# Kernel optimization log

Hardware: AMD Instinct MI355X
Metric: run time of the kernel (lower is better)

Reference implementation:

```python
import jax, jax.numpy as jnp
from jax import lax
import numpy as np

# inferred ssconv semantics (custom CUDA kernel not in source):
#  - input x: (B, H, W, Cin) channels-last, Cin = per-pixel channel count
#  - in_index: (B, H, W) in [0, IN_GROUPS): routes each input pixel's Cin channels
#    to the corresponding slice of the weight's input-channel dim (gather/scatter MoE-style dispatch)
#  - weight: (OUT_GROUPS*Cout, IN_GROUPS*Cin, kh, kw), bias: (OUT_GROUPS*Cout,)
#  - per output pixel, one out-group is selected (maxout over groups); the kernel
#    returns both the selected Cout channels and the winning group index (out_index)

IN_GROUPS = 4
OUT_GROUPS = 4
STRIDE = 1  # pad = stride//2 in the wrapper; output (H-1)//s+1 == SAME padding


def setup_inputs() -> dict:
    key = jax.random.key(0)
    k1, k2, k3, k4 = jax.random.split(key, 4)
    x = jax.random.normal(k1, (8, 256, 256, 16), dtype=jnp.float32)
    in_index = jax.random.randint(k2, (8, 256, 256), 0, IN_GROUPS, dtype=jnp.int32)
    weight = jax.random.normal(k3, (64, 64, 3, 3), dtype=jnp.float32) * 0.05
    bias = jax.random.normal(k4, (64,), dtype=jnp.float32) * 0.05
    return {"x": x, "in_index": in_index, "weight": weight, "bias": bias}


def reference(x, in_index, weight, bias):
    B, H, W, Cin = x.shape
    OC, IC, kh, kw = weight.shape  # OC = OUT_GROUPS*Cout, IC = IN_GROUPS*Cin
    Cout = OC // OUT_GROUPS

    # dispatch: scatter each pixel's channels into its in-group slice (rest zero)
    onehot = jax.nn.one_hot(in_index, IN_GROUPS, dtype=x.dtype)          # (B,H,W,G)
    x_full = (onehot[..., :, None] * x[..., None, :]).reshape(B, H, W, IN_GROUPS * Cin)

    # dense conv over the dispatched tensor == per-pixel gathered group weights
    w_hwio = jnp.transpose(weight, (2, 3, 1, 0))  # (kh,kw,IC,OC)
    out = lax.conv_general_dilated(
        x_full, w_hwio, window_strides=(STRIDE, STRIDE), padding="SAME",
        dimension_numbers=("NHWC", "HWIO", "NHWC"))
    out = out + bias  # (B,H',W',OC)

    Bo, Ho, Wo, _ = out.shape
    out_g = out.reshape(Bo, Ho, Wo, OUT_GROUPS, Cout)
    scores = out_g.max(axis=-1)                    # (B,H',W',G) per-group response
    out_index = jnp.argmax(scores, axis=-1)        # winning out-group per pixel
    sel = jnp.take_along_axis(out_g, out_index[..., None, None], axis=3)
    sel = jnp.squeeze(sel, axis=3)                 # (B,H',W',Cout)
    return sel, out_index.astype(jnp.int32)
```

## Files before the change

### kernel.cpp

```cpp
#include <hip/hip_runtime.h>

#define H 256
#define W 256
#define BATCH 8
#define CIN 16
#define TW 64
#define TH 4
#define HWC (TW + 2)
#define HHC (TH + 2)
#define NHALO (HWC * HHC)
#define PSTR 24
#define FIX_CAP 16384
#define GAP_TAU 1e-3f

#define OFF_HS   19008
#define OFF_GS   38016
#define OFF_BB   39600
#define SMEM_BYTES 72368

typedef __attribute__((ext_vector_type(8))) short short8;
typedef __attribute__((ext_vector_type(8))) _Float16 half8;
typedef __attribute__((ext_vector_type(4))) float f32x4;

union S8H8 { short8 s; half8 h; };
__device__ __forceinline__ half8 as_h8(short8 s) { S8H8 u; u.s = s; return u.h; }
union HU { _Float16 h; unsigned short u; };

__device__ __forceinline__ void gload_lds16(const void* g, void* l) {
    __builtin_amdgcn_global_load_lds(
        (const __attribute__((address_space(1))) unsigned int*)g,
        (__attribute__((address_space(3))) unsigned int*)l, 16, 0, 0);
}

__device__ __forceinline__ float4 add4(float4 a, float4 b) {
    return make_float4(a.x + b.x, a.y + b.y, a.z + b.z, a.w + b.w);
}
__device__ __forceinline__ float max4(float4 a) {
    return fmaxf(fmaxf(a.x, a.y), fmaxf(a.z, a.w));
}

__global__ void wprep_kernel(const float* __restrict__ w, unsigned short* __restrict__ wt) {
    int i = blockIdx.x * 256 + threadIdx.x;
    if (i >= 73728) return;
    int k   = i & 63;
    int n   = (i >> 6) & 63;
    int sel = (i >> 12) & 1;
    int tap = i >> 13;
    float v = w[(n * 64 + k) * 9 + tap] * 64.0f;
    HU uh; uh.h = (_Float16)v;
    unsigned short ob;
    if (sel == 0) {
        ob = uh.u;
    } else {
        _Float16 lo = (_Float16)((v - (float)uh.h) * 2048.0f);
        HU us; us.h = (_Float16)(uh.h + lo);
        ob = us.u;
    }
    int ksw = k ^ ((n & 7) << 3);
    wt[(((tap * 2 + sel) * 64) + n) * 64 + ksw] = ob;
}

#define CVT(F, VH, VS, J) { HU uh_; uh_.h = (_Float16)(F); \
    _Float16 lo_ = (_Float16)(((F) - (float)uh_.h) * 2048.0f); \
    HU us_; us_.h = (_Float16)(uh_.h + lo_); \
    VH[J] = (short)uh_.u; VS[J] = (short)us_.u; }

__global__ __launch_bounds__(256, 2) void ssconv_mfma_kernel(
    const float* __restrict__ x, const int* __restrict__ gidx,
    const unsigned short* __restrict__ wt, const float* __restrict__ bias,
    float* __restrict__ out_sel, float* __restrict__ out_idx,
    unsigned* __restrict__ fix_cnt, unsigned* __restrict__ fix_list)
{
    __shared__ __align__(16) char smem[SMEM_BYTES];
    unsigned short* hHi  = (unsigned short*)smem;
    unsigned short* hS   = (unsigned short*)(smem + OFF_HS);
    int* gsL             = (int*)(smem + OFF_GS);
    unsigned short* bufB = (unsigned short*)(smem + OFF_BB);
    float* outS          = (float*)smem;

    const int tid  = threadIdx.x;
    const int x0   = blockIdx.x * TW;
    const int y0   = blockIdx.y * TH;
    const int bz   = blockIdx.z;
    const int wvid = tid >> 6;
    const int L    = tid & 63;
    const int q    = L >> 4;
    const int lm   = L & 15;
    const int c0   = (q & 1) * 8;

#pragma unroll
    for (int c = 0; c < 4; ++c) {
        int seg = wvid * 4 + c;
        gload_lds16((const char*)wt + seg * 1024 + L * 16,
                    (char*)bufB + seg * 1024);
    }

    for (int i = tid; i < NHALO; i += 256) {
        int r = i / HWC, c = i % HWC;
        int hy = y0 + r - 1, hx = x0 + c - 1;
        bool ok = (hy >= 0) && (hy < H) && (hx >= 0) && (hx < W);
        float4 a0 = make_float4(0, 0, 0, 0), a1 = a0, a2 = a0, a3 = a0;
        int g = 0;
        if (ok) {
            const float4* src = (const float4*)(x + (((size_t)bz * H + hy) * W + hx) * CIN);
            a0 = src[0]; a1 = src[1]; a2 = src[2]; a3 = src[3];
            g = gidx[((size_t)bz * H + hy) * W + hx];
        }
        gsL[i] = g;
        short8 vh0, vs0, vh1, vs1;
        CVT(a0.x, vh0, vs0, 0) CVT(a0.y, vh0, vs0, 1) CVT(a0.z, vh0, vs0, 2) CVT(a0.w, vh0, vs0, 3)
        CVT(a1.x, vh0, vs0, 4) CVT(a1.y, vh0, vs0, 5) CVT(a1.z, vh0, vs0, 6) CVT(a1.w, vh0, vs0, 7)
        CVT(a2.x, vh1, vs1, 0) CVT(a2.y, vh1, vs1, 1) CVT(a2.z, vh1, vs1, 2) CVT(a2.w, vh1, vs1, 3)
        CVT(a3.x, vh1, vs1, 4) CVT(a3.y, vh1, vs1, 5) CVT(a3.z, vh1, vs1, 6) CVT(a3.w, vh1, vs1, 7)
        *(short8*)&hHi[i * PSTR + 0] = vh0;
        *(short8*)&hHi[i * PSTR + 8] = vh1;
        *(short8*)&hS[i * PSTR + 0]  = vs0;
        *(short8*)&hS[i * PSTR + 8]  = vs1;
    }
    __syncthreads();

    f32x4 acch[4][4] = {};
    f32x4 accc[4][4] = {};

#pragma unroll 1
    for (int tap = 0; tap < 9; ++tap) {
        if (tap < 8) {
            const char* gsrc = (const char*)(wt + (size_t)(tap + 1) * 8192);
            char* ldst = (char*)bufB + ((tap + 1) & 1) * 16384;
#pragma unroll
            for (int c = 0; c < 4; ++c) {
                int seg = wvid * 4 + c;
                gload_lds16(gsrc + seg * 1024 + L * 16, ldst + seg * 1024);
            }
        }
        const unsigned short* bb = bufB + (tap & 1) * 8192;

        const int dy = tap / 3, dx = tap % 3;
        const int hbase = (wvid + dy) * HWC + lm + dx;

        short8 ah[4], aS[4];
        int gg[4];
#pragma unroll
        for (int m = 0; m < 4; ++m) {
            int hb = hbase + 16 * m;
            gg[m] = gsL[hb];
            ah[m] = *(const short8*)&hHi[hb * PSTR + c0];
            aS[m] = *(const short8*)&hS[hb * PSTR + c0];
        }

#pragma unroll
        for (int ks = 0; ks < 2; ++ks) {
            const int gk = ks * 2 + (q >> 1);
            const int kcol = (ks * 32 + q * 8) ^ ((lm & 7) << 3);
            short8 bh[4], bt[4];
#pragma unroll
            for (int nt = 0; nt < 4; ++nt) {
                bh[nt] = *(const short8*)&bb[(nt * 16 + lm) * 64 + kcol];
                bt[nt] = *(const short8*)&bb[(64 + nt * 16 + lm) * 64 + kcol];
            }
            const short8 z = (short8)0;
#pragma unroll
            for (int m = 0; m < 4; ++m) {
                bool mm = (gg[m] == gk);
                short8 a0 = mm ? ah[m] : z;
                short8 s0 = mm ? aS[m] : z;
#pragma unroll
                for (int nt = 0; nt < 4; ++nt) {
                    acch[m][nt] = __builtin_amdgcn_mfma_f32_16x16x32_f16(as_h8(a0), as_h8(bh[nt]), acch[m][nt], 0, 0, 0);
                    accc[m][nt] = __builtin_amdgcn_mfma_f32_16x16x32_f16(as_h8(s0), as_h8(bt[nt]), accc[m][nt], 0, 0, 0);
                }
            }
        }
        __syncthreads();
    }

    const float SHm = 2047.0f / 131072.0f;
    const float SLc = 1.0f / 131072.0f;
#pragma unroll
    for (int m = 0; m < 4; ++m)
#pragma unroll
        for (int nt = 0; nt < 4; ++nt)
#pragma unroll
            for (int r = 0; r < 4; ++r) {
                int xcol = 16 * m + q * 4 + r;
                outS[wvid * 4352 + xcol * 68 + nt * 16 + lm] =
                    acch[m][nt][r] * SHm + accc[m][nt][r] * SLc;
            }
    __syncthreads();

#pragma unroll 1
    for (int pp = 0; pp < 2; ++pp) {
        int p  = (tid >> 1) + pp * 128;
        int hh = tid & 1;
        int pw = p >> 6, px_ = p & 63;
        const float4* srcp = (const float4*)(outS + pw * 4352 + px_ * 68 + hh * 32);
        const float4* bb2 = (const float4*)(bias + hh * 32);
        float4 r0 = add4(srcp[0], bb2[0]), r1 = add4(srcp[1], bb2[1]);
        float4 r2 = add4(srcp[2], bb2[2]), r3 = add4(srcp[3], bb2[3]);
        float4 r4 = add4(srcp[4], bb2[4]), r5 = add4(srcp[5], bb2[5]);
        float4 r6 = add4(srcp[6], bb2[6]), r7 = add4(srcp[7], bb2[7]);

        float ma = fmaxf(fmaxf(max4(r0), max4(r1)), fmaxf(max4(r2), max4(r3)));
        float mb = fmaxf(fmaxf(max4(r4), max4(r5)), fmaxf(max4(r6), max4(r7)));
        float pa = __shfl_xor(ma, 1, 64);
        float pb = __shfl_xor(mb, 1, 64);
        float s0, s1, s2, s3;
        if (hh == 0) { s0 = ma; s1 = mb; s2 = pa; s3 = pb; }
        else         { s0 = pa; s1 = pb; s2 = ma; s3 = mb; }
        int bg = 0; float best = s0;
        if (s1 > best) { best = s1; bg = 1; }
        if (s2 > best) { best = s2; bg = 2; }
        if (s3 > best) { best = s3; bg = 3; }

        int gy = y0 + pw, gx = x0 + px_;
        size_t opix = ((size_t)bz * H + gy) * W + gx;
        if ((bg >> 1) == hh) {
            bool useB = (bg & 1) != 0;
            float4 o0 = useB ? r4 : r0, o1 = useB ? r5 : r1;
            float4 o2 = useB ? r6 : r2, o3 = useB ? r7 : r3;
            float4* os = (float4*)(out_sel + opix * 16);
            os[0] = o0; os[1] = o1; os[2] = o2; os[3] = o3;
        }
        if (hh == 0) {
            out_idx[opix] = (float)bg;
            float o1v = (bg == 0) ? s1 : s0;
            float o2v = (bg <= 1) ? s2 : s1;
            float o3v = (bg <= 2) ? s3 : s2;
            float second = fmaxf(o1v, fmaxf(o2v, o3v));
            if (best - second < GAP_TAU) {
                unsigned slot = atomicAdd(fix_cnt, 1u);
                if (slot < FIX_CAP) fix_list[slot] = (unsigned)opix;
            }
        }
    }
}

__global__ void fixup_kernel(const float* __restrict__ x, const int* __restrict__ gidx,
                             const float* __restrict__ w, const float* __restrict__ bias,
                             float* __restrict__ out_sel, float* __restrict__ out_idx,
                             const unsigned* __restrict__ fix_cnt,
                             const unsigned* __restrict__ fix_list)
{
    unsigned n = *fix_cnt;
    if (n > FIX_CAP) n = FIX_CAP;
    const int lane = threadIdx.x & 63;
    const int nwaves = gridDim.x * (blockDim.x >> 6);
    unsigned widx = blockIdx.x * (blockDim.x >> 6) + (threadIdx.x >> 6);

    for (; widx < n; widx += nwaves) {
        unsigned opix = fix_list[widx];
        int b  = opix >> 16;
        int y  = (opix >> 8) & 255;
        int xc = opix & 255;
        double acc = (double)bias[lane];
        for (int dy = 0; dy < 3; ++dy) {
            int yy = y + dy - 1;
            if (yy < 0 || yy >= H) continue;
            for (int dx = 0; dx < 3; ++dx) {
                int xx = xc + dx - 1;
                if (xx < 0 || xx >= W) continue;
                size_t pix = ((size_t)b * H + yy) * W + xx;
                int g = gidx[pix];
                const float* xp = x + pix * 16;
                const float* wp = w + (size_t)(lane * 64 + g * 16) * 9 + (dy * 3 + dx);
#pragma unroll
                for (int c = 0; c < 16; ++c)
                    acc = fma((double)wp[c * 9], (double)xp[c], acc);
            }
        }
        double m = acc;
        m = fmax(m, __shfl_xor(m, 1, 64));
        m = fmax(m, __shfl_xor(m, 2, 64));
        m = fmax(m, __shfl_xor(m, 4, 64));
        m = fmax(m, __shfl_xor(m, 8, 64));
        double g0 = __shfl(m, 0, 64), g1 = __shfl(m, 16, 64);
        double g2 = __shfl(m, 32, 64), g3 = __shfl(m, 48, 64);
        int bg = 0; double bb = g0;
        if (g1 > bb) { bb = g1; bg = 1; }
        if (g2 > bb) { bb = g2; bg = 2; }
        if (g3 > bb) { bb = g3; bg = 3; }
        if ((lane >> 4) == bg) out_sel[(size_t)opix * 16 + (lane & 15)] = (float)acc;
        if (lane == 0) out_idx[opix] = (float)bg;
    }
}

extern "C" void kernel_launch(void* const* d_in, const int* in_sizes, int n_in,
                              void* d_out, int out_size, void* d_ws, size_t ws_size,
                              hipStream_t stream) {
    const float* x    = (const float*)d_in[0];
    const int*   gidx = (const int*)d_in[1];
    const float* w    = (const float*)d_in[2];
    const float* bias = (const float*)d_in[3];

    unsigned short* wt = (unsigned short*)d_ws;
    unsigned* fix_cnt  = (unsigned*)((char*)d_ws + 147456);
    unsigned* fix_list = (unsigned*)((char*)d_ws + 147472);

    float* out_sel = (float*)d_out;
    float* out_idx = (float*)d_out + (size_t)BATCH * H * W * CIN;

    hipMemsetAsync(fix_cnt, 0, 16, stream);
    wprep_kernel<<<288, 256, 0, stream>>>(w, wt);

    dim3 grid(W / TW, H / TH, BATCH);
    ssconv_mfma_kernel<<<grid, 256, 0, stream>>>(x, gidx, wt, bias, out_sel, out_idx,
                                                 fix_cnt, fix_list);
    fixup_kernel<<<256, 256, 0, stream>>>(x, gidx, w, bias, out_sel, out_idx,
                                          fix_cnt, fix_list);
}
```

Before: 189.0 us.

## Switch split-precision conv from fp16 MFMA to int8 hi/lo MFMA with per-tile scaling

Replaces the two-term fp16 decomposition with a two-term int8 quantization: weights get per-output-channel scales and activations get a per-tile absmax scale, and the conv runs on i32 16x16x64 int8 MFMA using three products (hi*hi, hi*lo, lo*hi). The tile height doubles to 8 rows with 512 threads, and all nine weight taps are preloaded into LDS at once instead of double-buffered. Group masking now uses a single K=64 step per tap. The memset is folded into the weight-prep kernel and the near-tie threshold is widened. The aim is to use the higher int8 MFMA throughput and cut LDS traffic, at the cost of accuracy and possibly more pixels sent to the fp64 fixup.

```diff
diff --git a/kernel.cpp b/kernel.cpp
--- a/kernel.cpp
+++ b/kernel.cpp
@@ -5,26 +5,22 @@
 #define BATCH 8
 #define CIN 16
 #define TW 64
-#define TH 4
+#define TH 8
 #define HWC (TW + 2)
 #define HHC (TH + 2)
 #define NHALO (HWC * HHC)
-#define PSTR 24
 #define FIX_CAP 16384
-#define GAP_TAU 1e-3f
-
-#define OFF_HS   19008
-#define OFF_GS   38016
-#define OFF_BB   39600
-#define SMEM_BYTES 72368
-
-typedef __attribute__((ext_vector_type(8))) short short8;
-typedef __attribute__((ext_vector_type(8))) _Float16 half8;
-typedef __attribute__((ext_vector_type(4))) float f32x4;
-
-union S8H8 { short8 s; half8 h; };
-__device__ __forceinline__ half8 as_h8(short8 s) { S8H8 u; u.s = s; return u.h; }
-union HU { _Float16 h; unsigned short u; };
+#define GAP_TAU 2e-3f
+
+#define OFF_XH   73728
+#define OFF_XL   84288
+#define OFF_GS   94848
+#define OFF_SW   97488
+#define OFF_BIAS 97744
+#define OFF_RED  98000
+#define SMEM_BYTES 98032
+
+typedef __attribute__((ext_vector_type(4))) int i32x4;
 
 __device__ __forceinline__ void gload_lds16(const void* g, void* l) {
     __builtin_amdgcn_global_load_lds(
@@ -39,44 +35,52 @@
     return fmaxf(fmaxf(a.x, a.y), fmaxf(a.z, a.w));
 }
 
-__global__ void wprep_kernel(const float* __restrict__ w, unsigned short* __restrict__ wt) {
-    int i = blockIdx.x * 256 + threadIdx.x;
-    if (i >= 73728) return;
-    int k   = i & 63;
-    int n   = (i >> 6) & 63;
-    int sel = (i >> 12) & 1;
-    int tap = i >> 13;
-    float v = w[(n * 64 + k) * 9 + tap] * 64.0f;
-    HU uh; uh.h = (_Float16)v;
-    unsigned short ob;
-    if (sel == 0) {
-        ob = uh.u;
-    } else {
-        _Float16 lo = (_Float16)((v - (float)uh.h) * 2048.0f);
-        HU us; us.h = (_Float16)(uh.h + lo);
-        ob = us.u;
-    }
-    int ksw = k ^ ((n & 7) << 3);
-    wt[(((tap * 2 + sel) * 64) + n) * 64 + ksw] = ob;
-}
-
-#define CVT(F, VH, VS, J) { HU uh_; uh_.h = (_Float16)(F); \
-    _Float16 lo_ = (_Float16)(((F) - (float)uh_.h) * 2048.0f); \
-    HU us_; us_.h = (_Float16)(uh_.h + lo_); \
-    VH[J] = (short)uh_.u; VS[J] = (short)us_.u; }
-
-__global__ __launch_bounds__(256, 2) void ssconv_mfma_kernel(
+__global__ void wprep_kernel(const float* __restrict__ w, char* __restrict__ wt,
+                             float* __restrict__ sw_ws, unsigned* __restrict__ fix_cnt) {
+    const int n = blockIdx.x;
+    const int k = threadIdx.x;
+    if (n == 0 && k == 0) fix_cnt[0] = 0u;
+
+    float v[9];
+    float m = 0.f;
+#pragma unroll
+    for (int t = 0; t < 9; ++t) {
+        v[t] = w[(n * 64 + k) * 9 + t];
+        m = fmaxf(m, fabsf(v[t]));
+    }
+#pragma unroll
+    for (int s = 1; s < 64; s <<= 1) m = fmaxf(m, __shfl_xor(m, s, 64));
+    const float inv = (m > 0.f) ? (127.f / m) : 0.f;
+    if (k == 0) sw_ws[n] = m * (1.f / 127.f);
+
+    const int nt = n >> 4, nl = n & 15, kq = k >> 4, j = k & 15;
+    const int lane16 = (kq * 16 + nl) * 16 + j;
+#pragma unroll
+    for (int t = 0; t < 9; ++t) {
+        float f = v[t] * inv;
+        int h = __float2int_rn(f);
+        int l = __float2int_rn((f - (float)h) * 128.f);
+        wt[((t * 2 + 0) * 4 + nt) * 1024 + lane16] = (char)h;
+        wt[((t * 2 + 1) * 4 + nt) * 1024 + lane16] = (char)l;
+    }
+}
+
+__global__ __launch_bounds__(512, 2) void ssconv_i8_kernel(
     const float* __restrict__ x, const int* __restrict__ gidx,
-    const unsigned short* __restrict__ wt, const float* __restrict__ bias,
+    const char* __restrict__ wt, const float* __restrict__ sw_ws,
+    const float* __restrict__ bias,
     float* __restrict__ out_sel, float* __restrict__ out_idx,
     unsigned* __restrict__ fix_cnt, unsigned* __restrict__ fix_list)
 {
     __shared__ __align__(16) char smem[SMEM_BYTES];
-    unsigned short* hHi  = (unsigned short*)smem;
-    unsigned short* hS   = (unsigned short*)(smem + OFF_HS);
-    int* gsL             = (int*)(smem + OFF_GS);
-    unsigned short* bufB = (unsigned short*)(smem + OFF_BB);
-    float* outS          = (float*)smem;
+    char*  bufB  = smem;
+    char*  xhL   = smem + OFF_XH;
+    char*  xlL   = smem + OFF_XL;
+    int*   gsL   = (int*)(smem + OFF_GS);
+    float* swdL  = (float*)(smem + OFF_SW);
+    float* biasL = (float*)(smem + OFF_BIAS);
+    float* redL  = (float*)(smem + OFF_RED);
+    float* outS  = (float*)smem;
 
     const int tid  = threadIdx.x;
     const int x0   = blockIdx.x * TW;
@@ -86,152 +90,172 @@
     const int L    = tid & 63;
     const int q    = L >> 4;
     const int lm   = L & 15;
-    const int c0   = (q & 1) * 8;
-
-#pragma unroll
-    for (int c = 0; c < 4; ++c) {
-        int seg = wvid * 4 + c;
-        gload_lds16((const char*)wt + seg * 1024 + L * 16,
-                    (char*)bufB + seg * 1024);
-    }
-
-    for (int i = tid; i < NHALO; i += 256) {
-        int r = i / HWC, c = i % HWC;
-        int hy = y0 + r - 1, hx = x0 + c - 1;
-        bool ok = (hy >= 0) && (hy < H) && (hx >= 0) && (hx < W);
-        float4 a0 = make_float4(0, 0, 0, 0), a1 = a0, a2 = a0, a3 = a0;
-        int g = 0;
-        if (ok) {
-            const float4* src = (const float4*)(x + (((size_t)bz * H + hy) * W + hx) * CIN);
-            a0 = src[0]; a1 = src[1]; a2 = src[2]; a3 = src[3];
-            g = gidx[((size_t)bz * H + hy) * W + hx];
-        }
-        gsL[i] = g;
-        short8 vh0, vs0, vh1, vs1;
-        CVT(a0.x, vh0, vs0, 0) CVT(a0.y, vh0, vs0, 1) CVT(a0.z, vh0, vs0, 2) CVT(a0.w, vh0, vs0, 3)
-        CVT(a1.x, vh0, vs0, 4) CVT(a1.y, vh0, vs0, 5) CVT(a1.z, vh0, vs0, 6) CVT(a1.w, vh0, vs0, 7)
-        CVT(a2.x, vh1, vs1, 0) CVT(a2.y, vh1, vs1, 1) CVT(a2.z, vh1, vs1, 2) CVT(a2.w, vh1, vs1, 3)
-        CVT(a3.x, vh1, vs1, 4) CVT(a3.y, vh1, vs1, 5) CVT(a3.z, vh1, vs1, 6) CVT(a3.w, vh1, vs1, 7)
-        *(short8*)&hHi[i * PSTR + 0] = vh0;
-        *(short8*)&hHi[i * PSTR + 8] = vh1;
-        *(short8*)&hS[i * PSTR + 0]  = vs0;
-        *(short8*)&hS[i * PSTR + 8]  = vs1;
-    }
+
+#pragma unroll
+    for (int it = 0; it < 9; ++it)
+        gload_lds16(wt + it * 8192 + tid * 16, bufB + it * 8192 + tid * 16);
+
+    if (tid < 64) { swdL[tid] = sw_ws[tid]; biasL[tid] = bias[tid]; }
+
+    float4 av[2][4];
+    int gv[2];
+    float am = 0.f;
+#pragma unroll
+    for (int s = 0; s < 2; ++s) {
+        av[s][0] = av[s][1] = av[s][2] = av[s][3] = make_float4(0, 0, 0, 0);
+        gv[s] = 0;
+        int i = tid + s * 512;
+        if (i < NHALO) {
+            int r = i / HWC, c = i - r * HWC;
+            int hy = y0 + r - 1, hx = x0 + c - 1;
+            if (hy >= 0 && hy < H && hx >= 0 && hx < W) {
+                const float4* src = (const float4*)(x + (((size_t)bz * H + hy) * W + hx) * CIN);
+                av[s][0] = src[0]; av[s][1] = src[1]; av[s][2] = src[2]; av[s][3] = src[3];
+                gv[s] = gidx[((size_t)bz * H + hy) * W + hx];
+            }
+#pragma unroll
+            for (int j = 0; j < 4; ++j)
+                am = fmaxf(am, fmaxf(fmaxf(fabsf(av[s][j].x), fabsf(av[s][j].y)),
+                                     fmaxf(fabsf(av[s][j].z), fabsf(av[s][j].w))));
+        }
+    }
+#pragma unroll
+    for (int s = 1; s < 64; s <<= 1) am = fmaxf(am, __shfl_xor(am, s, 64));
+    if (L == 0) redL[wvid] = am;
     __syncthreads();
-
-    f32x4 acch[4][4] = {};
-    f32x4 accc[4][4] = {};
+    float bm = redL[0];
+#pragma unroll
+    for (int wv = 1; wv < 8; ++wv) bm = fmaxf(bm, redL[wv]);
+    const float qinv = (bm > 0.f) ? (127.f / bm) : 0.f;
+    const float sB   = bm * (1.f / 127.f);
+
+#pragma unroll
+    for (int s = 0; s < 2; ++s) {
+        int i = tid + s * 512;
+        if (i < NHALO) {
+            unsigned hw[4], lw[4];
+#pragma unroll
+            for (int j = 0; j < 4; ++j) {
+                float fs[4] = {av[s][j].x, av[s][j].y, av[s][j].z, av[s][j].w};
+                unsigned hword = 0, lword = 0;
+#pragma unroll
+                for (int e = 0; e < 4; ++e) {
+                    float f_ = fs[e] * qinv;
+                    int h_ = __float2int_rn(f_);
+                    int l_ = __float2int_rn((f_ - (float)h_) * 128.f);
+                    hword |= ((unsigned)(h_ & 255)) << (8 * e);
+                    lword |= ((unsigned)(l_ & 255)) << (8 * e);
+                }
+                hw[j] = hword; lw[j] = lword;
+            }
+            *(uint4*)&xhL[(size_t)i * 16] = make_uint4(hw[0], hw[1], hw[2], hw[3]);
+            *(uint4*)&xlL[(size_t)i * 16] = make_uint4(lw[0], lw[1], lw[2], lw[3]);
+            gsL[i] = gv[s];
+        }
+    }
+    __syncthreads();
+
+    i32x4 acc1[4][4] = {};
+    i32x4 acc2[4][4] = {};
 
 #pragma unroll 1
     for (int tap = 0; tap < 9; ++tap) {
-        if (tap < 8) {
-            const char* gsrc = (const char*)(wt + (size_t)(tap + 1) * 8192);
-            char* ldst = (char*)bufB + ((tap + 1) & 1) * 16384;
-#pragma unroll
-            for (int c = 0; c < 4; ++c) {
-                int seg = wvid * 4 + c;
-                gload_lds16(gsrc + seg * 1024 + L * 16, ldst + seg * 1024);
-            }
-        }
-        const unsigned short* bb = bufB + (tap & 1) * 8192;
-
-        const int dy = tap / 3, dx = tap % 3;
+        const int dy = tap / 3, dx = tap - dy * 3;
         const int hbase = (wvid + dy) * HWC + lm + dx;
-
-        short8 ah[4], aS[4];
-        int gg[4];
+        const char* bB = bufB + tap * 8192;
+
+        i32x4 bh[4], bl[4];
+#pragma unroll
+        for (int nt = 0; nt < 4; ++nt) {
+            bh[nt] = *(const i32x4*)(bB + nt * 1024 + L * 16);
+            bl[nt] = *(const i32x4*)(bB + 4096 + nt * 1024 + L * 16);
+        }
 #pragma unroll
         for (int m = 0; m < 4; ++m) {
             int hb = hbase + 16 * m;
-            gg[m] = gsL[hb];
-            ah[m] = *(const short8*)&hHi[hb * PSTR + c0];
-            aS[m] = *(const short8*)&hS[hb * PSTR + c0];
-        }
-
-#pragma unroll
-        for (int ks = 0; ks < 2; ++ks) {
-            const int gk = ks * 2 + (q >> 1);
-            const int kcol = (ks * 32 + q * 8) ^ ((lm & 7) << 3);
-            short8 bh[4], bt[4];
+            int gg = gsL[hb];
+            i32x4 ah = *(const i32x4*)&xhL[(size_t)hb * 16];
+            i32x4 al = *(const i32x4*)&xlL[(size_t)hb * 16];
+            bool keep = (gg == q);
+            i32x4 z = {};
+            i32x4 a0 = keep ? ah : z;
+            i32x4 a1 = keep ? al : z;
 #pragma unroll
             for (int nt = 0; nt < 4; ++nt) {
-                bh[nt] = *(const short8*)&bb[(nt * 16 + lm) * 64 + kcol];
-                bt[nt] = *(const short8*)&bb[(64 + nt * 16 + lm) * 64 + kcol];
-            }
-            const short8 z = (short8)0;
-#pragma unroll
-            for (int m = 0; m < 4; ++m) {
-                bool mm = (gg[m] == gk);
-                short8 a0 = mm ? ah[m] : z;
-                short8 s0 = mm ? aS[m] : z;
-#pragma unroll
-                for (int nt = 0; nt < 4; ++nt) {
-                    acch[m][nt] = __builtin_amdgcn_mfma_f32_16x16x32_f16(as_h8(a0), as_h8(bh[nt]), acch[m][nt], 0, 0, 0);
-                    accc[m][nt] = __builtin_amdgcn_mfma_f32_16x16x32_f16(as_h8(s0), as_h8(bt[nt]), accc[m][nt], 0, 0, 0);
+                acc1[m][nt] = __builtin_amdgcn_mfma_i32_16x16x64_i8(a0, bh[nt], acc1[m][nt], 0, 0, 0);
+                acc2[m][nt] = __builtin_amdgcn_mfma_i32_16x16x64_i8(a0, bl[nt], acc2[m][nt], 0, 0, 0);
+                acc2[m][nt] = __builtin_amdgcn_mfma_i32_16x16x64_i8(a1, bh[nt], acc2[m][nt], 0, 0, 0);
+            }
+        }
+    }
+    __syncthreads();
+
+    float swb[4];
+#pragma unroll
+    for (int nt = 0; nt < 4; ++nt) swb[nt] = sB * swdL[nt * 16 + lm];
+
+#pragma unroll
+    for (int pass = 0; pass < 2; ++pass) {
+#pragma unroll
+        for (int mh = 0; mh < 2; ++mh) {
+            const int m = pass * 2 + mh;
+            const int prow = wvid * 32 + mh * 16 + q * 4;
+#pragma unroll
+            for (int nt = 0; nt < 4; ++nt)
+#pragma unroll
+                for (int r = 0; r < 4; ++r) {
+                    float v = swb[nt] *
+                              ((float)acc1[m][nt][r] + (float)acc2[m][nt][r] * (1.f / 128.f));
+                    outS[(prow + r) * 68 + nt * 16 + lm] = v;
                 }
-            }
         }
         __syncthreads();
-    }
-
-    const float SHm = 2047.0f / 131072.0f;
-    const float SLc = 1.0f / 131072.0f;
-#pragma unroll
-    for (int m = 0; m < 4; ++m)
-#pragma unroll
-        for (int nt = 0; nt < 4; ++nt)
-#pragma unroll
-            for (int r = 0; r < 4; ++r) {
-                int xcol = 16 * m + q * 4 + r;
-                outS[wvid * 4352 + xcol * 68 + nt * 16 + lm] =
-                    acch[m][nt][r] * SHm + accc[m][nt][r] * SLc;
-            }
-    __syncthreads();
-
-#pragma unroll 1
-    for (int pp = 0; pp < 2; ++pp) {
-        int p  = (tid >> 1) + pp * 128;
-        int hh = tid & 1;
-        int pw = p >> 6, px_ = p & 63;
-        const float4* srcp = (const float4*)(outS + pw * 4352 + px_ * 68 + hh * 32);
-        const float4* bb2 = (const float4*)(bias + hh * 32);
-        float4 r0 = add4(srcp[0], bb2[0]), r1 = add4(srcp[1], bb2[1]);
-        float4 r2 = add4(srcp[2], bb2[2]), r3 = add4(srcp[3], bb2[3]);
-        float4 r4 = add4(srcp[4], bb2[4]), r5 = add4(srcp[5], bb2[5]);
-        float4 r6 = add4(srcp[6], bb2[6]), r7 = add4(srcp[7], bb2[7]);
-
-        float ma = fmaxf(fmaxf(max4(r0), max4(r1)), fmaxf(max4(r2), max4(r3)));
-        float mb = fmaxf(fmaxf(max4(r4), max4(r5)), fmaxf(max4(r6), max4(r7)));
-        float pa = __shfl_xor(ma, 1, 64);
-        float pb = __shfl_xor(mb, 1, 64);
-        float s0, s1, s2, s3;
-        if (hh == 0) { s0 = ma; s1 = mb; s2 = pa; s3 = pb; }
-        else         { s0 = pa; s1 = pb; s2 = ma; s3 = mb; }
-        int bg = 0; float best = s0;
-        if (s1 > best) { best = s1; bg = 1; }
-        if (s2 > best) { best = s2; bg = 2; }
-        if (s3 > best) { best = s3; bg = 3; }
-
-        int gy = y0 + pw, gx = x0 + px_;
-        size_t opix = ((size_t)bz * H + gy) * W + gx;
-        if ((bg >> 1) == hh) {
-            bool useB = (bg & 1) != 0;
-            float4 o0 = useB ? r4 : r0, o1 = useB ? r5 : r1;
-            float4 o2 = useB ? r6 : r2, o3 = useB ? r7 : r3;
-            float4* os = (float4*)(out_sel + opix * 16);
-            os[0] = o0; os[1] = o1; os[2] = o2; os[3] = o3;
-        }
-        if (hh == 0) {
-            out_idx[opix] = (float)bg;
-            float o1v = (bg == 0) ? s1 : s0;
-            float o2v = (bg <= 1) ? s2 : s1;
-            float o3v = (bg <= 2) ? s3 : s2;
-            float second = fmaxf(o1v, fmaxf(o2v, o3v));
-            if (best - second < GAP_TAU) {
-                unsigned slot = atomicAdd(fix_cnt, 1u);
-                if (slot < FIX_CAP) fix_list[slot] = (unsigned)opix;
-            }
-        }
+
+        {
+            int p  = tid >> 1;
+            int hh = tid & 1;
+            const float4* srcp = (const float4*)(outS + p * 68 + hh * 32);
+            const float4* bb2  = (const float4*)(biasL + hh * 32);
+            float4 r0 = add4(srcp[0], bb2[0]), r1 = add4(srcp[1], bb2[1]);
+            float4 r2 = add4(srcp[2], bb2[2]), r3 = add4(srcp[3], bb2[3]);
+            float4 r4 = add4(srcp[4], bb2[4]), r5 = add4(srcp[5], bb2[5]);
+            float4 r6 = add4(srcp[6], bb2[6]), r7 = add4(srcp[7], bb2[7]);
+
+            float ma = fmaxf(fmaxf(max4(r0), max4(r1)), fmaxf(max4(r2), max4(r3)));
+            float mb = fmaxf(fmaxf(max4(r4), max4(r5)), fmaxf(max4(r6), max4(r7)));
+            float pa = __shfl_xor(ma, 1, 64);
+            float pb = __shfl_xor(mb, 1, 64);
+            float s0, s1, s2, s3;
+            if (hh == 0) { s0 = ma; s1 = mb; s2 = pa; s3 = pb; }
+            else         { s0 = pa; s1 = pb; s2 = ma; s3 = mb; }
+            int bg = 0; float best = s0;
+            if (s1 > best) { best = s1; bg = 1; }
+            if (s2 > best) { best = s2; bg = 2; }
+            if (s3 > best) { best = s3; bg = 3; }
+
+            int wv = p >> 5;
+            int gy = y0 + wv, gx = x0 + pass * 32 + (p & 31);
+            size_t opix = ((size_t)bz * H + gy) * W + gx;
+            if ((bg >> 1) == hh) {
+                bool useB = (bg & 1) != 0;
+                float4 o0 = useB ? r4 : r0, o1 = useB ? r5 : r1;
+                float4 o2 = useB ? r6 : r2, o3 = useB ? r7 : r3;
+                float4* os = (float4*)(out_sel + opix * 16);
+                os[0] = o0; os[1] = o1; os[2] = o2; os[3] = o3;
+            }
+            if (hh == 0) {
+                out_idx[opix] = (float)bg;
+                float o1v = (bg == 0) ? s1 : s0;
+                float o2v = (bg <= 1) ? s2 : s1;
+                float o3v = (bg <= 2) ? s3 : s2;
+                float second = fmaxf(o1v, fmaxf(o2v, o3v));
+                if (best - second < GAP_TAU) {
+                    unsigned slot = atomicAdd(fix_cnt, 1u);
+                    if (slot < FIX_CAP) fix_list[slot] = (unsigned)opix;
+                }
+            }
+        }
+        __syncthreads();
     }
 }
 
@@ -292,19 +316,19 @@
     const float* w    = (const float*)d_in[2];
     const float* bias = (const float*)d_in[3];
 
-    unsigned short* wt = (unsigned short*)d_ws;
-    unsigned* fix_cnt  = (unsigned*)((char*)d_ws + 147456);
-    unsigned* fix_list = (unsigned*)((char*)d_ws + 147472);
+    char*     wt       = (char*)d_ws;
+    float*    sw_ws    = (float*)((char*)d_ws + 73728);
+    unsigned* fix_cnt  = (unsigned*)((char*)d_ws + 73984);
+    unsigned* fix_list = (unsigned*)((char*)d_ws + 74000);
 
     float* out_sel = (float*)d_out;
     float* out_idx = (float*)d_out + (size_t)BATCH * H * W * CIN;
 
-    hipMemsetAsync(fix_cnt, 0, 16, stream);
-    wprep_kernel<<<288, 256, 0, stream>>>(w, wt);
+    wprep_kernel<<<64, 64, 0, stream>>>(w, wt, sw_ws, fix_cnt);
 
     dim3 grid(W / TW, H / TH, BATCH);
-    ssconv_mfma_kernel<<<grid, 256, 0, stream>>>(x, gidx, wt, bias, out_sel, out_idx,
-                                                 fix_cnt, fix_list);
+    ssconv_i8_kernel<<<grid, 512, 0, stream>>>(x, gidx, wt, sw_ws, bias,
+                                               out_sel, out_idx, fix_cnt, fix_list);
     fixup_kernel<<<256, 256, 0, stream>>>(x, gidx, w, bias, out_sel, out_idx,
                                           fix_cnt, fix_list);
 }
```

Measured after the change: 227.3 us. 20.2% more time.
